# Kernel tuning notes

Measured on AMD Instinct MI355X. Metric: run time of the kernel, lower is better.

Reference implementation:

```python
import jax, jax.numpy as jnp
import numpy as np

WIN = 7
NP_ = WIN * WIN
COV_NORM = NP_ / (NP_ - 1)

def _box(x, w):
    # valid 7x7 box filter, NCHW, single channel
    return jax.lax.conv_general_dilated(
        x, w, window_strides=(1, 1), padding='VALID',
        dimension_numbers=('NCHW', 'OIHW', 'NCHW'))

def setup_inputs() -> dict:
    key = jax.random.key(0)
    k1, k2, k3, k4 = jax.random.split(key, 4)
    N, H, W = 64, 384, 384
    X = jax.random.uniform(k1, (N, 1, H, W), dtype=jnp.float32)
    Y = jax.random.uniform(k2, (N, 1, H, W), dtype=jnp.float32)
    norm = jax.random.uniform(k3, (N,), dtype=jnp.float32)
    mx = jax.random.uniform(k4, (N,), dtype=jnp.float32) + 0.5
    w = jnp.ones((1, 1, WIN, WIN), dtype=jnp.float32) / NP_
    return {"X": X, "Y": Y, "norm": norm, "max": mx, "w": w}

def reference(X, Y, norm, max, w):
    q = 100000.0
    X = X * q
    Y = Y * q
    mx = max * q
    data_range = mx[:, None, None, None]
    C1 = (0.01 * data_range) ** 2
    C2 = (0.03 * data_range) ** 2
    ux = _box(X, w)
    uy = _box(Y, w)
    uxx = _box(X * X, w)
    uyy = _box(Y * Y, w)
    uxy = _box(X * Y, w)
    vx = COV_NORM * (uxx - ux * ux)
    vy = COV_NORM * (uyy - uy * uy)
    vxy = COV_NORM * (uxy - ux * uy)
    A1 = 2 * ux * uy + C1
    A2 = 2 * vxy + C2
    B1 = ux ** 2 + uy ** 2 + C1
    B2 = vx + vy + C2
    S = (A1 * A2) / (B1 * B2)
    return -jnp.mean(S)
```

## Files before the change

### kernel.cpp

```cpp
#include <hip/hip_runtime.h>


constexpr int IND   = 384;
constexpr int OUTD  = 378;
constexpr int RB    = 14;
constexpr int BANDS = OUTD / RB;
constexpr int CPL   = 6;

using f32x2 = __attribute__((ext_vector_type(2))) float;

__global__ __launch_bounds__(64, 2)
void ssim_band(const float* __restrict__ X, const float* __restrict__ Y,
               const float* __restrict__ MX, float* __restrict__ blocksum)
{
    const int band = blockIdx.x;
    const int n    = blockIdx.y;
    const int lane = threadIdx.x;
    const int c0   = lane * CPL;
    const int r0   = band * RB;

    const float* __restrict__ Xp = X + (size_t)n * (IND * IND) + c0;
    const float* __restrict__ Yp = Y + (size_t)n * (IND * IND) + c0;

    float hx[7][CPL], hy[7][CPL];
    float sx[CPL]  = {}, sy[CPL]  = {};
    float sxx[CPL] = {}, syy[CPL] = {}, sxy[CPL] = {};

#define LOADROW(DX, DY, R) {                                                  \
    const float* _px = Xp + (size_t)(R) * IND;                                \
    const float* _py = Yp + (size_t)(R) * IND;                                \
    f32x2 _a = *(const f32x2*)_px;                                            \
    f32x2 _b = *(const f32x2*)(_px + 2);                                      \
    f32x2 _c = *(const f32x2*)(_px + 4);                                      \
    f32x2 _d = *(const f32x2*)_py;                                            \
    f32x2 _e = *(const f32x2*)(_py + 2);                                      \
    f32x2 _f = *(const f32x2*)(_py + 4);                                      \
    DX[0]=_a.x; DX[1]=_a.y; DX[2]=_b.x; DX[3]=_b.y; DX[4]=_c.x; DX[5]=_c.y;   \
    DY[0]=_d.x; DY[1]=_d.y; DY[2]=_e.x; DY[3]=_e.y; DY[4]=_f.x; DY[5]=_f.y; }

#pragma unroll
    for (int k = 0; k < 7; ++k) LOADROW(hx[k], hy[k], r0 + k)

    float pax[CPL], pay[CPL], pbx[CPL], pby[CPL];
    LOADROW(pax, pay, r0 + 7)
    LOADROW(pbx, pby, r0 + 8)

#pragma unroll
    for (int k = 0; k < 7; ++k)
#pragma unroll
        for (int c = 0; c < CPL; ++c) {
            float x = hx[k][c], y = hy[k][c];
            sx[c] += x;  sy[c] += y;
            sxx[c] = fmaf(x, x, sxx[c]);
            syy[c] = fmaf(y, y, syy[c]);
            sxy[c] = fmaf(x, y, sxy[c]);
        }

    const float m   = MX[n];
    const float c1  = (0.01f * m) * (0.01f * m);
    const float c2  = (0.03f * m) * (0.03f * m);
    const float k1  = 2401.0f * c1;
    const float k2  = 2401.0f * c2;
    const float cn  = 49.0f / 48.0f;
    const float cn2 = 2.0f * cn;

#define HSUM(S, O) {                                                          \
    float _n0 = __shfl_down(S[0], 1), _n1 = __shfl_down(S[1], 1);             \
    float _n2 = __shfl_down(S[2], 1), _n3 = __shfl_down(S[3], 1);             \
    float _n4 = __shfl_down(S[4], 1), _n5 = __shfl_down(S[5], 1);             \
    float _t  = ((S[0]+S[1]) + (S[2]+S[3])) + (S[4]+S[5]);                    \
    O[0] = _t   + _n0;                                                        \
    O[1] = O[0] - S[0] + _n1;                                                 \
    O[2] = O[1] - S[1] + _n2;                                                 \
    O[3] = O[2] - S[2] + _n3;                                                 \
    O[4] = O[3] - S[3] + _n4;                                                 \
    O[5] = O[4] - S[4] + _n5; }

    float partial = 0.f;

#pragma unroll 1
    for (int kk = 0; kk < RB / 7; ++kk) {
#pragma unroll
        for (int i = 0; i < 7; ++i) {
            float t1[CPL], t2[CPL], t34[CPL], t5[CPL], u[CPL];
            HSUM(sx,  t1) HSUM(sy,  t2) HSUM(sxy, t5)
#pragma unroll
            for (int c = 0; c < CPL; ++c) u[c] = sxx[c] + syy[c];
            HSUM(u, t34)

            if (lane < 63) {
#pragma unroll
                for (int c = 0; c < CPL; ++c) {
                    float pxy = t1[c] * t2[c];
                    float ss  = fmaf(t1[c], t1[c], t2[c] * t2[c]);
                    float A1  = fmaf(2.f, pxy, k1);
                    float B1  = ss + k1;
                    float A2  = fmaf(cn2, fmaf(49.f, t5[c], -pxy), k2);
                    float B2  = fmaf(cn, fmaf(49.f, t34[c], -ss), k2);
                    partial += __fdividef(A1 * A2, B1 * B2);
                }
            }

#pragma unroll
            for (int c = 0; c < CPL; ++c) {
                float nx = pax[c], ny = pay[c];
                float ox = hx[i][c], oy = hy[i][c];
                sx[c] += nx - ox;
                sy[c] += ny - oy;
                sxx[c] = fmaf(nx, nx, fmaf(-ox, ox, sxx[c]));
                syy[c] = fmaf(ny, ny, fmaf(-oy, oy, syy[c]));
                sxy[c] = fmaf(nx, ny, fmaf(-ox, oy, sxy[c]));
                hx[i][c] = nx;  hy[i][c] = ny;
                pax[c] = pbx[c]; pay[c] = pby[c];
            }
            int nr = r0 + 7 * kk + i + 9;
            if (nr > IND - 1) nr = IND - 1;
            LOADROW(pbx, pby, nr)
        }
    }
#undef HSUM
#undef LOADROW

#pragma unroll
    for (int off = 32; off; off >>= 1) partial += __shfl_down(partial, off);
    if (lane == 0) blocksum[(size_t)n * BANDS + band] = partial;
}

__global__ __launch_bounds__(256)
void ssim_reduce(const float* __restrict__ blocksum, float* __restrict__ out,
                 int nblocks, float inv_npix)
{
    const int tid = threadIdx.x;
    float s = 0.f;
    for (int i = tid; i < nblocks; i += 256) s += blocksum[i];
#pragma unroll
    for (int off = 32; off; off >>= 1) s += __shfl_down(s, off);
    __shared__ float ws[4];
    if ((tid & 63) == 0) ws[tid >> 6] = s;
    __syncthreads();
    if (tid == 0) out[0] = -(ws[0] + ws[1] + ws[2] + ws[3]) * inv_npix;
}

extern "C" void kernel_launch(void* const* d_in, const int* in_sizes, int n_in,
                              void* d_out, int out_size, void* d_ws, size_t ws_size,
                              hipStream_t stream)
{
    const float* X  = (const float*)d_in[0];
    const float* Y  = (const float*)d_in[1];
    const float* MX = (const float*)d_in[3];

    const int N       = in_sizes[3];
    const int nblocks = N * BANDS;

    float* bs = (float*)d_ws;

    dim3 grid(BANDS, N);
    ssim_band<<<grid, 64, 0, stream>>>(X, Y, MX, bs);

    const float inv_npix = 1.0f / ((float)N * OUTD * OUTD);
    ssim_reduce<<<1, 256, 0, stream>>>(bs, (float*)d_out, nblocks, inv_npix);
}
```

Baseline: 28.45 us.

## Split each band into two column stripes with 4 columns per lane

Each image band is now split into two overlapping column stripes processed by separate blocks, so each lane owns 4 columns loaded as float4 instead of 6 columns as three float2 loads. The horizontal 7-wide sum is rebuilt around neighbour shuffles at distances 1 and 2, and the SSIM term is masked per column to avoid double counting in the overlap. This doubles the grid and raises the occupancy hint to 3 blocks per SIMD, aiming at more parallelism and fewer registers per thread. The cost is redundant loads in the overlap region, extra shuffles and per-column masking work.

```diff
diff --git a/kernel.cpp b/kernel.cpp
--- a/kernel.cpp
+++ b/kernel.cpp
@@ -1,42 +1,41 @@
 #include <hip/hip_runtime.h>
 
 
-constexpr int IND   = 384;
-constexpr int OUTD  = 378;
-constexpr int RB    = 14;
-constexpr int BANDS = OUTD / RB;
-constexpr int CPL   = 6;
+constexpr int IND    = 384;
+constexpr int OUTD   = 378;
+constexpr int RB     = 14;
+constexpr int BANDS  = OUTD / RB;
+constexpr int CPL    = 4;
+constexpr int SW     = 189;
 
-using f32x2 = __attribute__((ext_vector_type(2))) float;
+using f32x4 = __attribute__((ext_vector_type(4))) float;
 
-__global__ __launch_bounds__(64, 2)
+__global__ __launch_bounds__(64, 3)
 void ssim_band(const float* __restrict__ X, const float* __restrict__ Y,
                const float* __restrict__ MX, float* __restrict__ blocksum)
 {
-    const int band = blockIdx.x;
-    const int n    = blockIdx.y;
-    const int lane = threadIdx.x;
-    const int c0   = lane * CPL;
-    const int r0   = band * RB;
+    const int band   = blockIdx.x;
+    const int stripe = blockIdx.y;
+    const int n      = blockIdx.z;
+    const int lane   = threadIdx.x;
+    const int r0     = band * RB;
 
-    const float* __restrict__ Xp = X + (size_t)n * (IND * IND) + c0;
-    const float* __restrict__ Yp = Y + (size_t)n * (IND * IND) + c0;
+    const int c0  = (stripe == 0 ? 0 : 188) + lane * CPL;
+    int c0c = c0; if (c0c > IND - CPL) c0c = IND - CPL;
+    const int olo = stripe * SW;
+
+    const float* __restrict__ Xp = X + (size_t)n * (IND * IND) + c0c;
+    const float* __restrict__ Yp = Y + (size_t)n * (IND * IND) + c0c;
 
     float hx[7][CPL], hy[7][CPL];
     float sx[CPL]  = {}, sy[CPL]  = {};
     float sxx[CPL] = {}, syy[CPL] = {}, sxy[CPL] = {};
 
 #define LOADROW(DX, DY, R) {                                                  \
-    const float* _px = Xp + (size_t)(R) * IND;                                \
-    const float* _py = Yp + (size_t)(R) * IND;                                \
-    f32x2 _a = *(const f32x2*)_px;                                            \
-    f32x2 _b = *(const f32x2*)(_px + 2);                                      \
-    f32x2 _c = *(const f32x2*)(_px + 4);                                      \
-    f32x2 _d = *(const f32x2*)_py;                                            \
-    f32x2 _e = *(const f32x2*)(_py + 2);                                      \
-    f32x2 _f = *(const f32x2*)(_py + 4);                                      \
-    DX[0]=_a.x; DX[1]=_a.y; DX[2]=_b.x; DX[3]=_b.y; DX[4]=_c.x; DX[5]=_c.y;   \
-    DY[0]=_d.x; DY[1]=_d.y; DY[2]=_e.x; DY[3]=_e.y; DY[4]=_f.x; DY[5]=_f.y; }
+    f32x4 _a = *(const f32x4*)(Xp + (size_t)(R) * IND);                       \
+    f32x4 _b = *(const f32x4*)(Yp + (size_t)(R) * IND);                       \
+    DX[0]=_a.x; DX[1]=_a.y; DX[2]=_a.z; DX[3]=_a.w;                           \
+    DY[0]=_b.x; DY[1]=_b.y; DY[2]=_b.z; DY[3]=_b.w; }
 
 #pragma unroll
     for (int k = 0; k < 7; ++k) LOADROW(hx[k], hy[k], r0 + k)
@@ -64,17 +63,20 @@
     const float cn  = 49.0f / 48.0f;
     const float cn2 = 2.0f * cn;
 
-#define HSUM(S, O) {                                                          \
-    float _n0 = __shfl_down(S[0], 1), _n1 = __shfl_down(S[1], 1);             \
-    float _n2 = __shfl_down(S[2], 1), _n3 = __shfl_down(S[3], 1);             \
-    float _n4 = __shfl_down(S[4], 1), _n5 = __shfl_down(S[5], 1);             \
-    float _t  = ((S[0]+S[1]) + (S[2]+S[3])) + (S[4]+S[5]);                    \
-    O[0] = _t   + _n0;                                                        \
-    O[1] = O[0] - S[0] + _n1;                                                 \
-    O[2] = O[1] - S[1] + _n2;                                                 \
-    O[3] = O[2] - S[2] + _n3;                                                 \
-    O[4] = O[3] - S[3] + _n4;                                                 \
-    O[5] = O[4] - S[4] + _n5; }
+#define HSUM4(S, O) {                                                         \
+    float _p2 = S[0] + S[1];                                                  \
+    float _p3 = _p2 + S[2];                                                   \
+    float _T  = _p3 + S[3];                                                   \
+    float _n1p3 = __shfl_down(_p3, 1);                                        \
+    float _n1T  = __shfl_down(_T, 1);                                         \
+    float _n2p1 = __shfl_down(S[0], 2);                                       \
+    float _n2p2 = __shfl_down(_p2, 2);                                        \
+    float _sf2 = S[2] + S[3];                                                 \
+    float _sf1 = S[1] + _sf2;                                                 \
+    O[0] = _T   + _n1p3;                                                      \
+    O[1] = _sf1 + _n1T;                                                       \
+    O[2] = _sf2 + (_n1T + _n2p1);                                             \
+    O[3] = S[3] + (_n1T + _n2p2); }
 
     float partial = 0.f;
 
@@ -83,23 +85,10 @@
 #pragma unroll
         for (int i = 0; i < 7; ++i) {
             float t1[CPL], t2[CPL], t34[CPL], t5[CPL], u[CPL];
-            HSUM(sx,  t1) HSUM(sy,  t2) HSUM(sxy, t5)
+            HSUM4(sx,  t1) HSUM4(sy,  t2) HSUM4(sxy, t5)
 #pragma unroll
             for (int c = 0; c < CPL; ++c) u[c] = sxx[c] + syy[c];
-            HSUM(u, t34)
-
-            if (lane < 63) {
-#pragma unroll
-                for (int c = 0; c < CPL; ++c) {
-                    float pxy = t1[c] * t2[c];
-                    float ss  = fmaf(t1[c], t1[c], t2[c] * t2[c]);
-                    float A1  = fmaf(2.f, pxy, k1);
-                    float B1  = ss + k1;
-                    float A2  = fmaf(cn2, fmaf(49.f, t5[c], -pxy), k2);
-                    float B2  = fmaf(cn, fmaf(49.f, t34[c], -ss), k2);
-                    partial += __fdividef(A1 * A2, B1 * B2);
-                }
-            }
+            HSUM4(u, t34)
 
 #pragma unroll
             for (int c = 0; c < CPL; ++c) {
@@ -110,20 +99,37 @@
                 sxx[c] = fmaf(nx, nx, fmaf(-ox, ox, sxx[c]));
                 syy[c] = fmaf(ny, ny, fmaf(-oy, oy, syy[c]));
                 sxy[c] = fmaf(nx, ny, fmaf(-ox, oy, sxy[c]));
-                hx[i][c] = nx;  hy[i][c] = ny;
+                hx[i][c] = nx;   hy[i][c] = ny;
                 pax[c] = pbx[c]; pay[c] = pby[c];
             }
-            int nr = r0 + 7 * kk + i + 9;
-            if (nr > IND - 1) nr = IND - 1;
-            LOADROW(pbx, pby, nr)
+            {
+                int nr = r0 + 7 * kk + i + 9;
+                if (nr > IND - 1) nr = IND - 1;
+                LOADROW(pbx, pby, nr)
+            }
+
+#pragma unroll
+            for (int c = 0; c < CPL; ++c) {
+                int o = c0 + c;
+                if (o >= olo && o < olo + SW && o < OUTD) {
+                    float pxy = t1[c] * t2[c];
+                    float ss  = fmaf(t1[c], t1[c], t2[c] * t2[c]);
+                    float A1  = fmaf(2.f, pxy, k1);
+                    float B1  = ss + k1;
+                    float A2  = fmaf(cn2, fmaf(49.f, t5[c], -pxy), k2);
+                    float B2  = fmaf(cn, fmaf(49.f, t34[c], -ss), k2);
+                    partial += __fdividef(A1 * A2, B1 * B2);
+                }
+            }
         }
     }
-#undef HSUM
+#undef HSUM4
 #undef LOADROW
 
 #pragma unroll
     for (int off = 32; off; off >>= 1) partial += __shfl_down(partial, off);
-    if (lane == 0) blocksum[(size_t)n * BANDS + band] = partial;
+    if (lane == 0)
+        blocksum[((size_t)n * 2 + stripe) * BANDS + band] = partial;
 }
 
 __global__ __launch_bounds__(256)
@@ -150,11 +156,11 @@
     const float* MX = (const float*)d_in[3];
 
     const int N       = in_sizes[3];
-    const int nblocks = N * BANDS;
+    const int nblocks = N * 2 * BANDS;
 
     float* bs = (float*)d_ws;
 
-    dim3 grid(BANDS, N);
+    dim3 grid(BANDS, 2, N);
     ssim_band<<<grid, 64, 0, stream>>>(X, Y, MX, bs);
 
     const float inv_npix = 1.0f / ((float)N * OUTD * OUTD);
```

New measurement: 37.65 us. 1.32x slower.
